# Kernel optimization log

Hardware: AMD Instinct MI355X
Metric: run time of the kernel (lower is better)

Reference implementation:

```python
import jax, jax.numpy as jnp
import numpy as np

B, A, T, I, H = 256, 128, 50, 16, 128


def setup_inputs() -> dict:
    key = jax.random.key(0)
    k1, k2, k3, k4, k5 = jax.random.split(key, 5)
    bound = 1.0 / np.sqrt(H)
    sequence = jax.random.normal(k1, (B, A, T, I), dtype=jnp.float32)
    mask = jnp.ones((B, A, T), dtype=jnp.float32)
    # PyTorch LSTMCell params, gate order: input, forget, cell(g), output
    W_ih = jax.random.uniform(k2, (4 * H, I), minval=-bound, maxval=bound, dtype=jnp.float32)
    W_hh = jax.random.uniform(k3, (4 * H, H), minval=-bound, maxval=bound, dtype=jnp.float32)
    b_ih = jax.random.uniform(k4, (4 * H,), minval=-bound, maxval=bound, dtype=jnp.float32)
    b_hh = jax.random.uniform(k5, (4 * H,), minval=-bound, maxval=bound, dtype=jnp.float32)
    return {"sequence": sequence, "mask": mask, "W_ih": W_ih, "W_hh": W_hh, "b_ih": b_ih, "b_hh": b_hh}


def reference(sequence, mask, W_ih, W_hh, b_ih, b_hh):
    n_batch, n_agents, n_timesteps, _ = sequence.shape
    hidden_size = W_hh.shape[1]
    h0 = jnp.zeros((n_batch, n_agents, hidden_size), dtype=sequence.dtype)
    c0 = jnp.zeros((n_batch, n_agents, hidden_size), dtype=sequence.dtype)
    bias = b_ih + b_hh  # [4H]

    # time-major inputs for scan: [T, B, A, ...]
    seq_t = jnp.moveaxis(sequence, 2, 0)
    mask_t = jnp.moveaxis(mask, 2, 0)

    def step(carry, xs):
        h, c = carry
        x, m = xs  # x: [B, A, I], m: [B, A]
        gates = jnp.einsum('bai,gi->bag', x, W_ih) + jnp.einsum('bah,gh->bag', h, W_hh) + bias
        i_g, f_g, g_g, o_g = jnp.split(gates, 4, axis=-1)
        c_new = jax.nn.sigmoid(f_g) * c + jax.nn.sigmoid(i_g) * jnp.tanh(g_g)
        h_new = jax.nn.sigmoid(o_g) * jnp.tanh(c_new)
        m = m[..., None]  # [B, A, 1]
        h = m * h_new + (1.0 - m) * h
        c = m * c_new + (1.0 - m) * c
        return (h, c), None

    (h, c), _ = jax.lax.scan(step, (h0, c0), (seq_t, mask_t))
    return (h, c)
```

## Files before the change

kernel.cpp:

```cpp
#include <hip/hip_runtime.h>

#define T_ 50
#define I_ 16
#define H_ 128
#define S_ 32768
#define SPB 64
#define MT 4
#define ROWB 384

typedef _Float16 half8 __attribute__((ext_vector_type(8)));
typedef float f32x4 __attribute__((ext_vector_type(4)));

__device__ inline half8 h8zero() {
  half8 v;
#pragma unroll
  for (int j = 0; j < 8; ++j) v[j] = (_Float16)0.f;
  return v;
}

__global__ __launch_bounds__(512, 2)
void lstm_fused(const float* __restrict__ seq,
                const float* __restrict__ mask,
                const float* __restrict__ Wih,
                const float* __restrict__ Whh,
                const float* __restrict__ bih,
                const float* __restrict__ bhh,
                float* __restrict__ out)
{
  __shared__ char  hbuf[2][SPB * ROWB];
  __shared__ float mlds[SPB * T_];

  const int tid  = threadIdx.x;
  const int wav  = tid >> 6;
  const int lane = tid & 63;
  const int l15  = lane & 15;
  const int lg   = lane >> 4;
  const int sb   = blockIdx.x * SPB;

  const float L2E  = 1.44269504089f;
  const float L2E2 = 2.88539008178f;

  half8 wf[4][5];
  float nb[4];
#pragma unroll
  for (int n = 0; n < 4; ++n) {
    const int gate = 128 * n + 16 * wav + l15;
#pragma unroll
    for (int ks = 0; ks < 5; ++ks) {
      half8 f = h8zero();
#pragma unroll
      for (int j = 0; j < 8; ++j) {
        const int k = 32 * ks + 8 * lg + j;
        float v = 0.f;
        if (k < 128)      v = Whh[gate * 128 + k];
        else if (k < 144) v = Wih[gate * 16 + (k - 128)];
        f[j] = (_Float16)v;
      }
      wf[n][ks] = f;
    }
    const float bsum = bih[gate] + bhh[gate];
    nb[n] = (n == 2 ? -L2E2 : -L2E) * bsum;
  }

#pragma unroll
  for (int i = tid; i < SPB * T_; i += 512) mlds[i] = mask[(size_t)sb * T_ + i];

#pragma unroll
  for (int i = tid; i < 2 * SPB * ROWB / 16; i += 512) ((int4*)hbuf)[i] = make_int4(0, 0, 0, 0);

  float c_reg[MT][4];
  float h_reg[MT][4];
#pragma unroll
  for (int m = 0; m < MT; ++m)
#pragma unroll
    for (int r = 0; r < 4; ++r) { c_reg[m][r] = 0.f; h_reg[m][r] = 0.f; }

  const int xs  = tid >> 3;
  const int xi2 = (tid & 7) * 4;
  const float* xptr = seq + (size_t)(sb + xs) * (T_ * I_) + (tid & 7) * 2;
  const int xdst = xs * ROWB + ((256 + xi2) ^ ((xs & 7) << 4));

  {
    const float2 xv = *(const float2*)xptr;
    _Float16 hx[2] = {(_Float16)xv.x, (_Float16)xv.y};
    *(int*)&hbuf[0][xdst] = *(int*)hx;
  }
  __syncthreads();

#pragma unroll 1
  for (int t = 0; t < T_; ++t) {
    const int p = t & 1;
    const char* __restrict__ rd = hbuf[p];
    char* __restrict__       wr = hbuf[p ^ 1];

    float2 xv;
    if (t < T_ - 1) xv = *(const float2*)(xptr + (t + 1) * I_);

    f32x4 acc[MT][4];
#pragma unroll
    for (int m = 0; m < MT; ++m)
#pragma unroll
      for (int n = 0; n < 4; ++n) { f32x4 z = {0.f, 0.f, 0.f, 0.f}; acc[m][n] = z; }

#pragma unroll
    for (int m = 0; m < MT; ++m) {
      const int row = 16 * m + l15;
      const int swz = (row & 7) << 4;
      half8 a[5];
#pragma unroll
      for (int ks = 0; ks < 5; ++ks)
        a[ks] = *(const half8*)(rd + row * ROWB + ((64 * ks + 16 * lg) ^ swz));
#pragma unroll
      for (int n = 0; n < 4; ++n)
#pragma unroll
        for (int ks = 0; ks < 5; ++ks)
          acc[m][n] = __builtin_amdgcn_mfma_f32_16x16x32_f16(a[ks], wf[n][ks], acc[m][n], 0, 0, 0);
    }

#pragma unroll
    for (int m = 0; m < MT; ++m) {
#pragma unroll
      for (int r = 0; r < 4; ++r) {
        const int row = 16 * m + 4 * lg + r;
        const float iv = acc[m][0][r];
        const float fv = acc[m][1][r];
        const float gv = acc[m][2][r];
        const float ov = acc[m][3][r];
        const float ei = __builtin_amdgcn_exp2f(fminf(fmaf(iv, -L2E,  nb[0]), 30.f));
        const float ef = __builtin_amdgcn_exp2f(fminf(fmaf(fv, -L2E,  nb[1]), 30.f));
        const float eg = __builtin_amdgcn_exp2f(fminf(fmaf(gv, -L2E2, nb[2]), 30.f));
        const float eo = __builtin_amdgcn_exp2f(fminf(fmaf(ov, -L2E,  nb[3]), 30.f));
        const float pii = 1.f + ei, pif = 1.f + ef, pig = 1.f + eg, pio = 1.f + eo;
        const float mig = pii * pig;
        const float num = fmaf(c_reg[m][r], mig, (1.f - eg) * pif);
        const float cn  = num * __builtin_amdgcn_rcpf(mig * pif);
        const float ec  = __builtin_amdgcn_exp2f(fminf(cn * -L2E2, 30.f));
        const float hn  = (1.f - ec) * __builtin_amdgcn_rcpf(pio * (1.f + ec));
        const float mk = mlds[row * T_ + t];
        const float hN = fmaf(mk, hn - h_reg[m][r], h_reg[m][r]);
        const float cN = fmaf(mk, cn - c_reg[m][r], c_reg[m][r]);
        h_reg[m][r] = hN;
        c_reg[m][r] = cN;
        const int cb = (32 * wav + 2 * l15) ^ ((row & 7) << 4);
        *(_Float16*)(wr + row * ROWB + cb) = (_Float16)hN;
      }
    }

    if (t < T_ - 1) {
      _Float16 hx[2] = {(_Float16)xv.x, (_Float16)xv.y};
      *(int*)(wr + xdst) = *(int*)hx;
    }

    __syncthreads();
  }

#pragma unroll
  for (int m = 0; m < MT; ++m)
#pragma unroll
    for (int r = 0; r < 4; ++r) {
      const size_t s = (size_t)sb + 16 * m + 4 * lg + r;
      const int hc = 16 * wav + l15;
      out[s * H_ + hc] = h_reg[m][r];
      out[(size_t)S_ * H_ + s * H_ + hc] = c_reg[m][r];
    }
}

extern "C" void kernel_launch(void* const* d_in, const int* in_sizes, int n_in,
                              void* d_out, int out_size, void* d_ws, size_t ws_size,
                              hipStream_t stream) {
  const float* seq  = (const float*)d_in[0];
  const float* mask = (const float*)d_in[1];
  const float* Wih  = (const float*)d_in[2];
  const float* Whh  = (const float*)d_in[3];
  const float* bih  = (const float*)d_in[4];
  const float* bhh  = (const float*)d_in[5];
  float* out = (float*)d_out;
  lstm_fused<<<dim3(S_ / SPB), dim3(512), 0, stream>>>(seq, mask, Wih, Whh, bih, bhh, out);
}
```

Before: 513.2 us.

## Software-pipeline MFMA tiles with gate updates and precompute LDS offsets

Restructures the per-timestep loop so the matrix multiply for the next 16-row tile runs while the gate nonlinearities of the previous tile are computed, using two alternating accumulator sets. LDS addresses are precomputed once and ping-ponged with XOR toggles instead of being recomputed each step. The mask is stored time-major so each lane reads its four mask values with one vector load. The aim is to hide MFMA latency behind transcendental VALU work and cut address arithmetic, at the cost of extra live registers that may pressure the two-blocks-per-CU occupancy target.

```diff
diff --git a/kernel.cpp b/kernel.cpp
--- a/kernel.cpp
+++ b/kernel.cpp
@@ -7,6 +7,8 @@
 #define SPB 64
 #define MT 4
 #define ROWB 384
+#define BSTR 32768
+#define MOFF (2*BSTR)
 
 typedef _Float16 half8 __attribute__((ext_vector_type(8)));
 typedef float f32x4 __attribute__((ext_vector_type(4)));
@@ -27,8 +29,7 @@
                 const float* __restrict__ bhh,
                 float* __restrict__ out)
 {
-  __shared__ char  hbuf[2][SPB * ROWB];
-  __shared__ float mlds[SPB * T_];
+  __shared__ char lds[MOFF + T_ * SPB * 4];
 
   const int tid  = threadIdx.x;
   const int wav  = tid >> 6;
@@ -58,15 +59,18 @@
       }
       wf[n][ks] = f;
     }
-    const float bsum = bih[gate] + bhh[gate];
-    nb[n] = (n == 2 ? -L2E2 : -L2E) * bsum;
-  }
-
-#pragma unroll
-  for (int i = tid; i < SPB * T_; i += 512) mlds[i] = mask[(size_t)sb * T_ + i];
-
-#pragma unroll
-  for (int i = tid; i < 2 * SPB * ROWB / 16; i += 512) ((int4*)hbuf)[i] = make_int4(0, 0, 0, 0);
+    nb[n] = (n == 2 ? -L2E2 : -L2E) * (bih[gate] + bhh[gate]);
+  }
+
+  {
+    const int s = tid >> 3;
+    const float* mp = mask + (size_t)(sb + s) * T_;
+#pragma unroll 1
+    for (int t = tid & 7; t < T_; t += 8)
+      *(float*)(lds + MOFF + t * 256 + s * 4) = mp[t];
+  }
+#pragma unroll 1
+  for (int i = tid; i < 2 * BSTR / 16; i += 512) ((int4*)lds)[i] = make_int4(0, 0, 0, 0);
 
   float c_reg[MT][4];
   float h_reg[MT][4];
@@ -75,83 +79,102 @@
 #pragma unroll
     for (int r = 0; r < 4; ++r) { c_reg[m][r] = 0.f; h_reg[m][r] = 0.f; }
 
-  const int xs  = tid >> 3;
-  const int xi2 = (tid & 7) * 4;
-  const float* xptr = seq + (size_t)(sb + xs) * (T_ * I_) + (tid & 7) * 2;
-  const int xdst = xs * ROWB + ((256 + xi2) ^ ((xs & 7) << 4));
-
+  int rdo[5];
+  const int swzr = (l15 & 7) << 4;
+#pragma unroll
+  for (int ks = 0; ks < 5; ++ks) rdo[ks] = l15 * ROWB + ((64 * ks + 16 * lg) ^ swzr);
+  int wro[4];
+#pragma unroll
+  for (int r = 0; r < 4; ++r) {
+    const int row = 4 * lg + r;
+    wro[r] = BSTR + row * ROWB + ((32 * wav + 2 * l15) ^ ((row & 7) << 4));
+  }
+  const int xs = tid >> 3, xq = tid & 7;
+  int xwo = BSTR + xs * ROWB + ((256 + 4 * xq) ^ ((xs & 7) << 4));
+  int mo  = MOFF + 16 * lg;
+
+  const float* xptr = seq + (size_t)(sb + xs) * (T_ * I_) + 2 * xq;
+
+  __syncthreads();
   {
     const float2 xv = *(const float2*)xptr;
     _Float16 hx[2] = {(_Float16)xv.x, (_Float16)xv.y};
-    *(int*)&hbuf[0][xdst] = *(int*)hx;
+    *(int*)(lds + (xwo ^ BSTR)) = *(int*)hx;
   }
   __syncthreads();
+
+  auto loadA = [&](half8* a, int mb) {
+#pragma unroll
+    for (int ks = 0; ks < 5; ++ks)
+      a[ks] = *(const half8*)(lds + (rdo[ks] + mb));
+  };
+  auto runM = [&](const half8* a, f32x4* ac) {
+#pragma unroll
+    for (int ks = 0; ks < 5; ++ks)
+#pragma unroll
+      for (int n = 0; n < 4; ++n)
+        ac[n] = __builtin_amdgcn_mfma_f32_16x16x32_f16(a[ks], wf[n][ks], ac[n], 0, 0, 0);
+  };
+  auto zero4 = [&](f32x4* ac) {
+    f32x4 z = {0.f, 0.f, 0.f, 0.f};
+    ac[0] = z; ac[1] = z; ac[2] = z; ac[3] = z;
+  };
+  auto updM = [&](int m, const f32x4* ac) {
+    const f32x4 mv = *(const f32x4*)(lds + (mo + 64 * m));
+#pragma unroll
+    for (int r = 0; r < 4; ++r) {
+      const float iv = ac[0][r], fv = ac[1][r], gv = ac[2][r], ov = ac[3][r];
+      const float ei = __builtin_amdgcn_exp2f(fminf(fmaf(iv, -L2E,  nb[0]), 30.f));
+      const float ef = __builtin_amdgcn_exp2f(fminf(fmaf(fv, -L2E,  nb[1]), 30.f));
+      const float eg = __builtin_amdgcn_exp2f(fminf(fmaf(gv, -L2E2, nb[2]), 30.f));
+      const float eo = __builtin_amdgcn_exp2f(fminf(fmaf(ov, -L2E,  nb[3]), 30.f));
+      const float pii = 1.f + ei, pif = 1.f + ef, pig = 1.f + eg, pio = 1.f + eo;
+      const float mig = pii * pig;
+      const float num = fmaf(c_reg[m][r], mig, (1.f - eg) * pif);
+      const float cn  = num * __builtin_amdgcn_rcpf(mig * pif);
+      const float ec  = __builtin_amdgcn_exp2f(fminf(cn * -L2E2, 30.f));
+      const float hn  = (1.f - ec) * __builtin_amdgcn_rcpf(pio * (1.f + ec));
+      const float mk  = mv[r];
+      const float hN  = fmaf(mk, hn - h_reg[m][r], h_reg[m][r]);
+      const float cN  = fmaf(mk, cn - c_reg[m][r], c_reg[m][r]);
+      h_reg[m][r] = hN;
+      c_reg[m][r] = cN;
+      *(_Float16*)(lds + (wro[r] + 6144 * m)) = (_Float16)hN;
+    }
+  };
 
 #pragma unroll 1
   for (int t = 0; t < T_; ++t) {
-    const int p = t & 1;
-    const char* __restrict__ rd = hbuf[p];
-    char* __restrict__       wr = hbuf[p ^ 1];
-
     float2 xv;
     if (t < T_ - 1) xv = *(const float2*)(xptr + (t + 1) * I_);
 
-    f32x4 acc[MT][4];
-#pragma unroll
-    for (int m = 0; m < MT; ++m)
-#pragma unroll
-      for (int n = 0; n < 4; ++n) { f32x4 z = {0.f, 0.f, 0.f, 0.f}; acc[m][n] = z; }
-
-#pragma unroll
-    for (int m = 0; m < MT; ++m) {
-      const int row = 16 * m + l15;
-      const int swz = (row & 7) << 4;
-      half8 a[5];
-#pragma unroll
-      for (int ks = 0; ks < 5; ++ks)
-        a[ks] = *(const half8*)(rd + row * ROWB + ((64 * ks + 16 * lg) ^ swz));
-#pragma unroll
-      for (int n = 0; n < 4; ++n)
-#pragma unroll
-        for (int ks = 0; ks < 5; ++ks)
-          acc[m][n] = __builtin_amdgcn_mfma_f32_16x16x32_f16(a[ks], wf[n][ks], acc[m][n], 0, 0, 0);
-    }
-
-#pragma unroll
-    for (int m = 0; m < MT; ++m) {
-#pragma unroll
-      for (int r = 0; r < 4; ++r) {
-        const int row = 16 * m + 4 * lg + r;
-        const float iv = acc[m][0][r];
-        const float fv = acc[m][1][r];
-        const float gv = acc[m][2][r];
-        const float ov = acc[m][3][r];
-        const float ei = __builtin_amdgcn_exp2f(fminf(fmaf(iv, -L2E,  nb[0]), 30.f));
-        const float ef = __builtin_amdgcn_exp2f(fminf(fmaf(fv, -L2E,  nb[1]), 30.f));
-        const float eg = __builtin_amdgcn_exp2f(fminf(fmaf(gv, -L2E2, nb[2]), 30.f));
-        const float eo = __builtin_amdgcn_exp2f(fminf(fmaf(ov, -L2E,  nb[3]), 30.f));
-        const float pii = 1.f + ei, pif = 1.f + ef, pig = 1.f + eg, pio = 1.f + eo;
-        const float mig = pii * pig;
-        const float num = fmaf(c_reg[m][r], mig, (1.f - eg) * pif);
-        const float cn  = num * __builtin_amdgcn_rcpf(mig * pif);
-        const float ec  = __builtin_amdgcn_exp2f(fminf(cn * -L2E2, 30.f));
-        const float hn  = (1.f - ec) * __builtin_amdgcn_rcpf(pio * (1.f + ec));
-        const float mk = mlds[row * T_ + t];
-        const float hN = fmaf(mk, hn - h_reg[m][r], h_reg[m][r]);
-        const float cN = fmaf(mk, cn - c_reg[m][r], c_reg[m][r]);
-        h_reg[m][r] = hN;
-        c_reg[m][r] = cN;
-        const int cb = (32 * wav + 2 * l15) ^ ((row & 7) << 4);
-        *(_Float16*)(wr + row * ROWB + cb) = (_Float16)hN;
-      }
-    }
+    half8 aA[5], aB[5];
+    f32x4 acA[4], acB[4];
+    loadA(aA, 0);
+    loadA(aB, 6144);
+    zero4(acA); runM(aA, acA);
+    loadA(aA, 12288);
+    zero4(acB); runM(aB, acB);
+    updM(0, acA);
+    zero4(acA); runM(aA, acA);
+    loadA(aB, 18432);
+    updM(1, acB);
+    zero4(acB); runM(aB, acB);
+    updM(2, acA);
+    updM(3, acB);
 
     if (t < T_ - 1) {
       _Float16 hx[2] = {(_Float16)xv.x, (_Float16)xv.y};
-      *(int*)(wr + xdst) = *(int*)hx;
+      *(int*)(lds + xwo) = *(int*)hx;
     }
 
     __syncthreads();
+#pragma unroll
+    for (int ks = 0; ks < 5; ++ks) rdo[ks] ^= BSTR;
+#pragma unroll
+    for (int r = 0; r < 4; ++r) wro[r] ^= BSTR;
+    xwo ^= BSTR;
+    mo += 256;
   }
 
 #pragma unroll
```

New measurement: 477.0 us. -7.0%, faster.
